# Kernel tuning notes

Hardware: AMD Instinct MI355X
Metric: run time of the kernel (lower is better)

The kernel has to match this reference:

```python
import jax, jax.numpy as jnp
import numpy as np

H1 = 768
H2 = 768
B, LQ, LK = 8, 1024, 1024


def setup_inputs() -> dict:
    key = jax.random.key(0)
    ks = jax.random.split(key, 12)
    s1 = 1.0 / np.sqrt(H1)
    s2 = 1.0 / np.sqrt(H2)
    # weights stored as [in, out] (equivalent to torch Linear weight.T)
    return {
        "tensor1": jax.random.normal(ks[0], (B, LQ, H1), jnp.float32),
        "tensor2": jax.random.normal(ks[1], (B, LK, H2), jnp.float32),
        "Wq": jax.random.uniform(ks[2], (3, H1, H2), jnp.float32, -s1, s1),
        "bq": jax.random.uniform(ks[3], (3, H2), jnp.float32, -s1, s1),
        "Wk": jax.random.uniform(ks[4], (3, H2, H2), jnp.float32, -s2, s2),
        "bk": jax.random.uniform(ks[5], (3, H2), jnp.float32, -s2, s2),
        "Wv": jax.random.uniform(ks[6], (3, H2, H2), jnp.float32, -s2, s2),
        "bv": jax.random.uniform(ks[7], (3, H2), jnp.float32, -s2, s2),
        "Wp": jax.random.uniform(ks[8], (3 * H2, H2), jnp.float32, -1.0 / np.sqrt(3 * H2), 1.0 / np.sqrt(3 * H2)),
        "bp": jax.random.uniform(ks[9], (H2,), jnp.float32, -1.0 / np.sqrt(3 * H2), 1.0 / np.sqrt(3 * H2)),
    }


def reference(tensor1, tensor2, Wq, bq, Wk, bk, Wv, bv, Wp, bp):
    # Three independent cross-attention heads, stacked on leading axis h=3.
    q = jnp.einsum("bqd,hde->hbqe", tensor1, Wq) + bq[:, None, None, :]  # [3,B,LQ,H2]
    k = jnp.einsum("bkd,hde->hbke", tensor2, Wk) + bk[:, None, None, :]  # [3,B,LK,H2]
    v = jnp.einsum("bkd,hde->hbke", tensor2, Wv) + bv[:, None, None, :]  # [3,B,LK,H2]
    scores = jnp.einsum("hbqe,hbke->hbqk", q, k)  # NOTE: no 1/sqrt(d) scaling, per original
    weights = jax.nn.softmax(scores, axis=-1)
    ctx = jnp.einsum("hbqk,hbke->hbqe", weights, v)  # [3,B,LQ,H2]
    # concat heads along feature dim -> [B,LQ,3*H2]
    multi = jnp.transpose(ctx, (1, 2, 0, 3)).reshape(ctx.shape[1], ctx.shape[2], -1)
    # project_multihead: ReLU then Linear
    return jax.nn.relu(multi) @ Wp + bp
```

## Files before the change

kernel.cpp:

```cpp
#include <hip/hip_runtime.h>
#include <hip/hip_bf16.h>


typedef _Float16 f16;
typedef __attribute__((ext_vector_type(8))) _Float16 f16x8;
typedef __attribute__((ext_vector_type(4))) float f32x4;
typedef __attribute__((ext_vector_type(4))) short s16x4;

#define DI __device__ __forceinline__

DI short f2hs(float f){
  f16 h = (f16)f;
  return __builtin_bit_cast(short, h);
}
DI float hs2f(short s){
  return (float)__builtin_bit_cast(f16, s);
}

DI f32x4 mfma16(f16x8 a, f16x8 b, f32x4 c){
  return __builtin_amdgcn_mfma_f32_16x16x32_f16(a, b, c, 0, 0, 0);
}

#define GLL16(gp, lp) __builtin_amdgcn_global_load_lds( \
    (const __attribute__((address_space(1))) unsigned int*)(gp), \
    (__attribute__((address_space(3))) unsigned int*)(lp), 16, 0, 0)

__global__ void cvt2_f16_kernel(const float* __restrict__ a, const float* __restrict__ b,
                                short* __restrict__ oa, short* __restrict__ ob, int n4each){
  int i = blockIdx.x * blockDim.x + threadIdx.x;
  const float* in = (i < n4each) ? a : b;
  short* out = (i < n4each) ? oa : ob;
  int j = (i < n4each) ? i : i - n4each;
  f32x4 v = ((const f32x4*)in)[j];
  s16x4 o;
  o[0]=f2hs(v[0]); o[1]=f2hs(v[1]); o[2]=f2hs(v[2]); o[3]=f2hs(v[3]);
  ((s16x4*)out)[j] = o;
}

__global__ void transpose2_kernel(const float* __restrict__ Wv, const float* __restrict__ Wp,
                                  short* __restrict__ WvT, short* __restrict__ WpT){
  __shared__ float tile[32][33];
  const float* in; short* out; int R, r0;
  if (blockIdx.z == 0){
    int hd = blockIdx.y / 24;
    in = Wv + (long)hd*768*768; out = WvT + (long)hd*768*768;
    R = 768; r0 = (blockIdx.y % 24) * 32;
  } else {
    in = Wp; out = WpT; R = 2304; r0 = blockIdx.y * 32;
  }
  int c0 = blockIdx.x * 32;
  int tx = threadIdx.x, ty = threadIdx.y;
  #pragma unroll
  for (int k=0;k<4;k++)
    tile[ty + k*8][tx] = in[(long)(r0 + ty + k*8) * 768 + c0 + tx];
  __syncthreads();
  #pragma unroll
  for (int k=0;k<4;k++)
    out[(long)(c0 + ty + k*8) * R + r0 + tx] = f2hs(tile[tx][ty + k*8]);
}

DI void gemm_tile64(const short* __restrict__ A, const short* __restrict__ Bt, int K,
                    int m0, int n0, short* As, short* Bs, f32x4 (&acc)[4][4])
{
  const int tid = threadIdx.x, wave = tid>>6, lane = tid&63;
  const int wm = wave>>1, wn = wave&1;
  const int fl = lane&15, fq = lane>>4;
  const int srow = lane>>2, scol = (lane&3)*8;
  for (int kk=0; kk<K; kk+=64){
    __syncthreads();
    #pragma unroll
    for (int c=0;c<2;c++)
      #pragma unroll
      for (int r=0;r<2;r++){
        const int rb = r*64 + wave*16;
        GLL16(A  + (long)(m0+rb+srow)*K + kk + c*32 + scol, As + c*4096 + rb*32);
        GLL16(Bt + (long)(n0+rb+srow)*K + kk + c*32 + scol, Bs + c*4096 + rb*32);
      }
    __syncthreads();
    #pragma unroll
    for (int c=0;c<2;c++){
      f16x8 a[4];
      #pragma unroll
      for (int i=0;i<4;i++) a[i] = *(const f16x8*)(As + c*4096 + (wm*64+i*16+fl)*32 + fq*8);
      #pragma unroll
      for (int j=0;j<4;j++){
        f16x8 b = *(const f16x8*)(Bs + c*4096 + (wn*64+j*16+fl)*32 + fq*8);
        #pragma unroll
        for (int i=0;i<4;i++) acc[i][j] = mfma16(a[i], b, acc[i][j]);
      }
    }
  }
}

__global__ __launch_bounds__(256,2) void gemm_m_kernel(
    const short* __restrict__ WqH, const short* __restrict__ WkH, short* __restrict__ Mt)
{
  __shared__ short As[8192];
  __shared__ short Bs[8192];
  const int h = blockIdx.z;
  const int m0 = blockIdx.x*128, n0 = blockIdx.y*128;
  const int tid = threadIdx.x, wave = tid>>6, lane = tid&63;
  const int wm = wave>>1, wn = wave&1;
  const int fl = lane&15, fq = lane>>4;

  f32x4 vz = {0.f,0.f,0.f,0.f};
  f32x4 acc[4][4];
  #pragma unroll
  for (int i=0;i<4;i++)
    #pragma unroll
    for (int j=0;j<4;j++) acc[i][j] = vz;

  gemm_tile64(WqH + (long)h*768*768, WkH + (long)h*768*768, 768, m0, n0, As, Bs, acc);

  short* outp = Mt + (long)h*768*768;
  #pragma unroll
  for (int j=0;j<4;j++){
    int col = n0 + wn*64 + j*16 + fl;
    #pragma unroll
    for (int i=0;i<4;i++){
      int row = m0 + wm*64 + i*16 + fq*4;
      s16x4 pack;
      #pragma unroll
      for (int r=0;r<4;r++) pack[r] = f2hs(acc[i][j][r]);
      *(s16x4*)(outp + (long)col*768 + row) = pack;
    }
  }
}

__global__ void vvec_kernel(const float* __restrict__ Wk, const float* __restrict__ bq,
                            float* __restrict__ w){
  const int h = blockIdx.x, chunk = blockIdx.y;
  const int tid = threadIdx.x, wave = tid>>6, lane = tid&63;
  const float* bql = bq + h*768 + lane*12;
  float bv[12];
  #pragma unroll
  for (int e=0;e<12;e++) bv[e] = bql[e];
  for (int r = 0; r < 24; r++){
    int d = chunk*96 + r*4 + wave;
    const float* row = Wk + ((long)h*768 + d)*768 + lane*12;
    float s = 0.f;
    #pragma unroll
    for (int e=0;e<12;e++) s += row[e] * bv[e];
    s += __shfl_xor(s, 1);
    s += __shfl_xor(s, 2);
    s += __shfl_xor(s, 4);
    s += __shfl_xor(s, 8);
    s += __shfl_xor(s, 16);
    s += __shfl_xor(s, 32);
    if (lane == 0) w[h*768 + d] = s;
  }
}

__global__ __launch_bounds__(256,2) void gemm_gv_kernel(
    const short* __restrict__ t1b, const short* __restrict__ t2b,
    const short* __restrict__ Mt, const short* __restrict__ WvT,
    const float* __restrict__ wv, const float* __restrict__ bv,
    short* __restrict__ Gb, short* __restrict__ Vtb)
{
  __shared__ short As[8192];
  __shared__ short Bs[8192];
  const int z = blockIdx.z;
  const int h = z % 3, which = z / 3;
  const short* A  = (which==0) ? t1b : t2b;
  const short* Bt = ((which==0)?Mt:WvT) + (long)h*768*768;
  const int m0 = blockIdx.x*128, n0 = blockIdx.y*128;
  const int tid = threadIdx.x, wave = tid>>6, lane = tid&63;
  const int wm = wave>>1, wn = wave&1;
  const int fl = lane&15, fq = lane>>4;

  f32x4 vz = {0.f,0.f,0.f,0.f};
  f32x4 acc[4][4];
  #pragma unroll
  for (int i=0;i<4;i++)
    #pragma unroll
    for (int j=0;j<4;j++) acc[i][j] = vz;

  gemm_tile64(A, Bt, 768, m0, n0, As, Bs, acc);

  if (which == 0){
    const float* bias = wv + h*768;
    short* outp = Gb + (long)h*8192*768;
    #pragma unroll
    for (int j=0;j<4;j++){
      int col = n0 + wn*64 + j*16 + fl;
      float bb = bias[col];
      #pragma unroll
      for (int i=0;i<4;i++){
        int row = m0 + wm*64 + i*16 + fq*4;
        #pragma unroll
        for (int r=0;r<4;r++)
          outp[(long)(row+r)*768 + col] = f2hs(acc[i][j][r] + bb);
      }
    }
  } else {
    const float* bias = bv + h*768;
    const int bidx = m0 >> 10;
    const int lk0  = m0 & 1023;
    short* outp = Vtb + (long)(h*8 + bidx)*768*1024;
    #pragma unroll
    for (int j=0;j<4;j++){
      int e = n0 + wn*64 + j*16 + fl;
      float bb = bias[e];
      #pragma unroll
      for (int i=0;i<4;i++){
        int lk = lk0 + wm*64 + i*16 + fq*4;
        s16x4 pack;
        #pragma unroll
        for (int r=0;r<4;r++) pack[r] = f2hs(acc[i][j][r] + bb);
        *(s16x4*)(outp + (long)e*1024 + lk) = pack;
      }
    }
  }
}

__global__ __launch_bounds__(256,2) void qk_exp_kernel(
    const short* __restrict__ Gb, const short* __restrict__ t2b,
    short* __restrict__ P, float* __restrict__ Mx, float* __restrict__ Lx)
{
  __shared__ short As[8192];
  __shared__ short Bs[8192];
  __shared__ float red0[2][2][64];
  __shared__ float red1[2][2][64];
  const int id = blockIdx.x;
  const int xcd = id & 7, s_ = id >> 3;
  const int hb = xcd*3 + (s_ >> 6);
  const int inner = s_ & 63;
  const int qt = inner & 7, ct = inner >> 3;
  const int h = hb >> 3, b = hb & 7;
  const int tid = threadIdx.x, wave = tid>>6, lane = tid&63;
  const int wm = wave>>1, wn = wave&1;
  const int fl = lane&15, fq = lane>>4;
  const short* Abase = Gb + ((long)h*8192 + b*1024)*768;
  const short* Bbase = t2b + (long)b*1024*768;

  f32x4 vz = {0.f,0.f,0.f,0.f};
  f32x4 acc[4][4];
  #pragma unroll
  for (int i=0;i<4;i++)
    #pragma unroll
    for (int j=0;j<4;j++) acc[i][j] = vz;

  gemm_tile64(Abase, Bbase, 768, qt*128, ct*128, As, Bs, acc);

  float mt[4][4];
  #pragma unroll
  for (int i=0;i<4;i++)
    #pragma unroll
    for (int r=0;r<4;r++){
      float m = acc[i][0][r];
      #pragma unroll
      for (int j=1;j<4;j++) m = fmaxf(m, acc[i][j][r]);
      m = fmaxf(m, __shfl_xor(m, 1));
      m = fmaxf(m, __shfl_xor(m, 2));
      m = fmaxf(m, __shfl_xor(m, 4));
      m = fmaxf(m, __shfl_xor(m, 8));
      mt[i][r] = m;
      if (fl == 0) red0[wn][wm][i*16 + fq*4 + r] = m;
    }
  __syncthreads();
  #pragma unroll
  for (int i=0;i<4;i++)
    #pragma unroll
    for (int r=0;r<4;r++)
      mt[i][r] = fmaxf(red0[0][wm][i*16 + fq*4 + r], red0[1][wm][i*16 + fq*4 + r]);

  #pragma unroll
  for (int i=0;i<4;i++)
    #pragma unroll
    for (int r=0;r<4;r++){
      float s = 0.f;
      #pragma unroll
      for (int j=0;j<4;j++){
        float p = __expf(acc[i][j][r] - mt[i][r]);
        acc[i][j][r] = p;
        s += p;
      }
      s += __shfl_xor(s, 1);
      s += __shfl_xor(s, 2);
      s += __shfl_xor(s, 4);
      s += __shfl_xor(s, 8);
      if (fl == 0) red1[wn][wm][i*16 + fq*4 + r] = s;
    }
  __syncthreads();

  #pragma unroll
  for (int j=0;j<4;j++){
    int c = ct*128 + wn*64 + j*16 + fl;
    #pragma unroll
    for (int i=0;i<4;i++){
      int q = qt*128 + wm*64 + i*16 + fq*4;
      #pragma unroll
      for (int r=0;r<4;r++)
        P[((long)hb*1024 + q + r)*1024 + c] = f2hs(acc[i][j][r]);
    }
  }
  if (fl == 0 && wn == 0){
    long aux = ((long)(hb*8 + ct))*1024 + qt*128;
    #pragma unroll
    for (int i=0;i<4;i++)
      #pragma unroll
      for (int r=0;r<4;r++){
        int row = wm*64 + i*16 + fq*4 + r;
        Mx[aux + row] = mt[i][r];
        Lx[aux + row] = red1[0][wm][row & 63] + red1[1][wm][row & 63];
      }
  }
}

__global__ __launch_bounds__(256,2) void pv_kernel(
    const short* __restrict__ P, const short* __restrict__ Vtb,
    const float* __restrict__ Mx, const float* __restrict__ Lx, short* __restrict__ multi)
{
  __shared__ short As[8192];
  __shared__ short Bs[8192];
  __shared__ float scl[8][128];
  const int id = blockIdx.x;
  const int xcd = id & 7, s_ = id >> 3;
  const int hb = xcd*3 + s_/48;
  const int inner = s_ % 48;
  const int qt = inner & 7, et = inner >> 3;
  const int h = hb >> 3, b = hb & 7;
  const int tid = threadIdx.x, wave = tid>>6, lane = tid&63;
  const int wm = wave>>1, wn = wave&1;
  const int fl = lane&15, fq = lane>>4;
  const int srow = lane>>2, scol = (lane&3)*8;
  const short* Abase = P + (long)hb*1024*1024 + (long)(qt*128)*1024;
  const short* Bbase = Vtb + (long)hb*768*1024 + (long)(et*128)*1024;

  if (tid < 128){
    long a0 = ((long)(hb*8))*1024 + qt*128 + tid;
    float m[8], l[8];
    #pragma unroll
    for (int t=0;t<8;t++){ m[t] = Mx[a0 + t*1024]; l[t] = Lx[a0 + t*1024]; }
    float mg = m[0];
    #pragma unroll
    for (int t=1;t<8;t++) mg = fmaxf(mg, m[t]);
    float lg = 0.f;
    #pragma unroll
    for (int t=0;t<8;t++) lg += l[t] * __expf(m[t] - mg);
    float inv = 1.0f / lg;
    #pragma unroll
    for (int t=0;t<8;t++) scl[t][tid] = __expf(m[t] - mg) * inv;
  }
  __syncthreads();

  f32x4 vz = {0.f,0.f,0.f,0.f};
  f32x4 acc[4][4];
  #pragma unroll
  for (int i=0;i<4;i++)
    #pragma unroll
    for (int j=0;j<4;j++) acc[i][j] = vz;

  for (int ct=0; ct<8; ct++){
    f16 s[4];
    #pragma unroll
    for (int i=0;i<4;i++) s[i] = (f16)scl[ct][wm*64 + i*16 + fl];
    #pragma unroll
    for (int t=0;t<2;t++){
      const int kk = ct*128 + t*64;
      __syncthreads();
      #pragma unroll
      for (int c=0;c<2;c++)
        #pragma unroll
        for (int r=0;r<2;r++){
          const int rb = r*64 + wave*16;
          GLL16(Abase + (long)(rb+srow)*1024 + kk + c*32 + scol, As + c*4096 + rb*32);
          GLL16(Bbase + (long)(rb+srow)*1024 + kk + c*32 + scol, Bs + c*4096 + rb*32);
        }
      __syncthreads();
      #pragma unroll
      for (int c=0;c<2;c++){
        f16x8 a[4];
        #pragma unroll
        for (int i=0;i<4;i++){
          f16x8 av = *(const f16x8*)(As + c*4096 + (wm*64+i*16+fl)*32 + fq*8);
          f16x8 sv;
          #pragma unroll
          for (int e=0;e<8;e++) sv[e] = s[i];
          a[i] = av * sv;
        }
        #pragma unroll
        for (int j=0;j<4;j++){
          f16x8 bvv = *(const f16x8*)(Bs + c*4096 + (wn*64+j*16+fl)*32 + fq*8);
          #pragma unroll
          for (int i=0;i<4;i++) acc[i][j] = mfma16(a[i], bvv, acc[i][j]);
        }
      }
    }
  }

  short* mp = multi + (long)(b*1024 + qt*128)*2304 + h*768 + et*128;
  #pragma unroll
  for (int j=0;j<4;j++){
    int e = wn*64 + j*16 + fl;
    #pragma unroll
    for (int i=0;i<4;i++){
      int q = wm*64 + i*16 + fq*4;
      #pragma unroll
      for (int r=0;r<4;r++)
        mp[(long)(q+r)*2304 + e] = f2hs(fmaxf(acc[i][j][r], 0.f));
    }
  }
}

__global__ __launch_bounds__(256,2) void gemm_out_kernel(
    const short* __restrict__ A, const short* __restrict__ Bt,
    const float* __restrict__ bias, float* __restrict__ out)
{
  __shared__ short As[8192];
  __shared__ short Bs[8192];
  const int m0 = blockIdx.x*128, n0 = blockIdx.y*128;
  const int tid = threadIdx.x, wave = tid>>6, lane = tid&63;
  const int wm = wave>>1, wn = wave&1;
  const int fl = lane&15, fq = lane>>4;

  f32x4 vz = {0.f,0.f,0.f,0.f};
  f32x4 acc[4][4];
  #pragma unroll
  for (int i=0;i<4;i++)
    #pragma unroll
    for (int j=0;j<4;j++) acc[i][j] = vz;

  gemm_tile64(A, Bt, 2304, m0, n0, As, Bs, acc);

  #pragma unroll
  for (int j=0;j<4;j++){
    int col = n0 + wn*64 + j*16 + fl;
    float bb = bias[col];
    #pragma unroll
    for (int i=0;i<4;i++){
      int row = m0 + wm*64 + i*16 + fq*4;
      #pragma unroll
      for (int r=0;r<4;r++)
        out[(long)(row+r)*768 + col] = acc[i][j][r] + bb;
    }
  }
}

extern "C" void kernel_launch(void* const* d_in, const int* in_sizes, int n_in,
                              void* d_out, int out_size, void* d_ws, size_t ws_size,
                              hipStream_t stream)
{
  const float* t1 = (const float*)d_in[0];
  const float* t2 = (const float*)d_in[1];
  const float* Wq = (const float*)d_in[2];
  const float* bq = (const float*)d_in[3];
  const float* Wk = (const float*)d_in[4];
  const float* Wv = (const float*)d_in[6];
  const float* bv = (const float*)d_in[7];
  const float* Wp = (const float*)d_in[8];
  const float* bp = (const float*)d_in[9];
  float* out = (float*)d_out;

  char* ws = (char*)d_ws;
  size_t off = 0;
  auto carve = [&](size_t bytes){ void* p = ws + off; off += (bytes + 255) & ~(size_t)255; return p; };
  short* t1b = (short*)carve(8L*1024*768*2);
  short* t2b = (short*)carve(8L*1024*768*2);
  short* WqH = (short*)carve(3L*768*768*2);
  short* WkH = (short*)carve(3L*768*768*2);
  short* WvT = (short*)carve(3L*768*768*2);
  short* WpT = (short*)carve(768L*2304*2);
  short* Mt  = (short*)carve(3L*768*768*2);
  short* Gb  = (short*)carve(3L*8192*768*2);
  short* Vtb = (short*)carve(3L*8*768*1024*2);
  short* Pb  = (short*)carve(24L*1024*1024*2);
  float* Mx  = (float*)carve(24L*8*1024*4);
  float* Lx  = (float*)carve(24L*8*1024*4);
  float* wvb = (float*)carve(3L*768*4);
  short* multib = Gb;

  cvt2_f16_kernel<<<12288, 256, 0, stream>>>(t1, t2, t1b, t2b, 1572864);
  cvt2_f16_kernel<<<3456, 256, 0, stream>>>(Wq, Wk, WqH, WkH, 442368);
  transpose2_kernel<<<dim3(24,72,2), dim3(32,8), 0, stream>>>(Wv, Wp, WvT, WpT);
  vvec_kernel<<<dim3(3,8), 256, 0, stream>>>(Wk, bq, wvb);
  gemm_m_kernel<<<dim3(6,6,3), 256, 0, stream>>>(WqH, WkH, Mt);
  gemm_gv_kernel<<<dim3(64,6,6), 256, 0, stream>>>(t1b, t2b, Mt, WvT, wvb, bv, Gb, Vtb);
  qk_exp_kernel<<<1536, 256, 0, stream>>>(Gb, t2b, Pb, Mx, Lx);
  pv_kernel<<<1152, 256, 0, stream>>>(Pb, Vtb, Mx, Lx, multib);
  gemm_out_kernel<<<dim3(64,6,1), 256, 0, stream>>>(multib, WpT, bp, out);
}
```

Baseline: 399.4 us.

## Use 256x256 tiles with 4-stage async LDS pipeline in G/V projection GEMM

Replaces the 128x128 tile G/V projection GEMM with a 512-thread 256x256 tile kernel. Each wave now computes a 128x64 sub-tile. Operands are loaded into LDS through a 4-deep ring of direct global-to-LDS loads with XOR swizzling, explicit vmcnt waits and raised MFMA priority. The larger tiles raise arithmetic intensity and the prefetch hides load latency, at the cost of more LDS (128KB per block) and more registers, plus fewer blocks (576) to spread across CUs.

```diff
diff --git a/kernel.cpp b/kernel.cpp
--- a/kernel.cpp
+++ b/kernel.cpp
@@ -151,31 +151,85 @@
   }
 }
 
-__global__ __launch_bounds__(256,2) void gemm_gv_kernel(
+__global__ __launch_bounds__(512,2) void gemm_gv256_kernel(
     const short* __restrict__ t1b, const short* __restrict__ t2b,
     const short* __restrict__ Mt, const short* __restrict__ WvT,
     const float* __restrict__ wv, const float* __restrict__ bv,
     short* __restrict__ Gb, short* __restrict__ Vtb)
 {
-  __shared__ short As[8192];
-  __shared__ short Bs[8192];
+  __shared__ short As4[4][8192];
+  __shared__ short Bs4[4][8192];
+
   const int z = blockIdx.z;
   const int h = z % 3, which = z / 3;
   const short* A  = (which==0) ? t1b : t2b;
   const short* Bt = ((which==0)?Mt:WvT) + (long)h*768*768;
-  const int m0 = blockIdx.x*128, n0 = blockIdx.y*128;
-  const int tid = threadIdx.x, wave = tid>>6, lane = tid&63;
-  const int wm = wave>>1, wn = wave&1;
+  const int m0 = blockIdx.x*256, n0 = blockIdx.y*256;
+  const int tid = threadIdx.x, wave = tid>>6, lane = tid&63;
+  const int wm = wave>>2, wn = wave&3;
   const int fl = lane&15, fq = lane>>4;
 
+  const int lr = lane>>2;
+  const int ss = ((lane&3) ^ ((lane>>3)&3)) * 8;
+  const int rs = (fq ^ ((fl>>1)&3)) * 8;
+
   f32x4 vz = {0.f,0.f,0.f,0.f};
-  f32x4 acc[4][4];
-  #pragma unroll
-  for (int i=0;i<4;i++)
+  f32x4 acc[8][4];
+  #pragma unroll
+  for (int i=0;i<8;i++)
     #pragma unroll
     for (int j=0;j<4;j++) acc[i][j] = vz;
 
-  gemm_tile64(A, Bt, 768, m0, n0, As, Bs, acc);
+  auto STAGE = [&](int rg, int s){
+    const int kk = s*32;
+    #pragma unroll
+    for (int g=0; g<2; g++){
+      const int rb = g*128 + wave*16;
+      GLL16(A  + (long)(m0+rb+lr)*768 + kk + ss, &As4[rg][rb*32]);
+      GLL16(Bt + (long)(n0+rb+lr)*768 + kk + ss, &Bs4[rg][rb*32]);
+    }
+  };
+
+  auto COMPUTE = [&](int rg){
+    const short* Ab = &As4[rg][0];
+    const short* Bb = &Bs4[rg][0];
+    f16x8 b[4];
+    #pragma unroll
+    for (int j=0;j<4;j++)
+      b[j] = *(const f16x8*)(Bb + (wn*64 + j*16 + fl)*32 + rs);
+    #pragma unroll
+    for (int mq=0; mq<2; mq++){
+      f16x8 a[4];
+      #pragma unroll
+      for (int i=0;i<4;i++)
+        a[i] = *(const f16x8*)(Ab + (wm*128 + mq*64 + i*16 + fl)*32 + rs);
+      __builtin_amdgcn_s_setprio(1);
+      #pragma unroll
+      for (int j=0;j<4;j++)
+        #pragma unroll
+        for (int i=0;i<4;i++)
+          acc[mq*4+i][j] = mfma16(a[i], b[j], acc[mq*4+i][j]);
+      __builtin_amdgcn_s_setprio(0);
+    }
+  };
+
+  STAGE(0, 0);
+  STAGE(1, 1);
+  asm volatile("s_waitcnt vmcnt(4)" ::: "memory");
+  __builtin_amdgcn_s_barrier();
+
+  for (int s = 0; s < 22; ++s){
+    STAGE((s+2)&3, s+2);
+    asm volatile("s_waitcnt vmcnt(8)" ::: "memory");
+    __builtin_amdgcn_s_barrier();
+    COMPUTE(s&3);
+  }
+  asm volatile("s_waitcnt vmcnt(4)" ::: "memory");
+  __builtin_amdgcn_s_barrier();
+  COMPUTE(22&3);
+  asm volatile("s_waitcnt vmcnt(0)" ::: "memory");
+  __builtin_amdgcn_s_barrier();
+  COMPUTE(23&3);
 
   if (which == 0){
     const float* bias = wv + h*768;
@@ -185,8 +239,8 @@
       int col = n0 + wn*64 + j*16 + fl;
       float bb = bias[col];
       #pragma unroll
-      for (int i=0;i<4;i++){
-        int row = m0 + wm*64 + i*16 + fq*4;
+      for (int i=0;i<8;i++){
+        int row = m0 + wm*128 + i*16 + fq*4;
         #pragma unroll
         for (int r=0;r<4;r++)
           outp[(long)(row+r)*768 + col] = f2hs(acc[i][j][r] + bb);
@@ -202,8 +256,8 @@
       int e = n0 + wn*64 + j*16 + fl;
       float bb = bias[e];
       #pragma unroll
-      for (int i=0;i<4;i++){
-        int lk = lk0 + wm*64 + i*16 + fq*4;
+      for (int i=0;i<8;i++){
+        int lk = lk0 + wm*128 + i*16 + fq*4;
         s16x4 pack;
         #pragma unroll
         for (int r=0;r<4;r++) pack[r] = f2hs(acc[i][j][r] + bb);
@@ -475,7 +529,7 @@
   transpose2_kernel<<<dim3(24,72,2), dim3(32,8), 0, stream>>>(Wv, Wp, WvT, WpT);
   vvec_kernel<<<dim3(3,8), 256, 0, stream>>>(Wk, bq, wvb);
   gemm_m_kernel<<<dim3(6,6,3), 256, 0, stream>>>(WqH, WkH, Mt);
-  gemm_gv_kernel<<<dim3(64,6,6), 256, 0, stream>>>(t1b, t2b, Mt, WvT, wvb, bv, Gb, Vtb);
+  gemm_gv256_kernel<<<dim3(32,3,6), 512, 0, stream>>>(t1b, t2b, Mt, WvT, wvb, bv, Gb, Vtb);
   qk_exp_kernel<<<1536, 256, 0, stream>>>(Gb, t2b, Pb, Mx, Lx);
   pv_kernel<<<1152, 256, 0, stream>>>(Pb, Vtb, Mx, Lx, multib);
   gemm_out_kernel<<<dim3(64,6,1), 256, 0, stream>>>(multib, WpT, bp, out);
```

Measured after the change: 413.3 us. 3.5% more time.

## Fuse preprocessing kernels into one launch and XOR-swizzle LDS tiles

Applied to the files above, without the earlier changes.

Merges the four preprocessing kernels (activation and weight casts, the Wv/Wp transposes, and the bias-vector reduction) into one block-indexed launch to cut launch gaps and tail effects. It also applies an XOR swizzle to the LDS column chunk, both in the global_load_lds writes and in the fragment reads of gemm_tile64 and pv_kernel, to reduce LDS bank conflicts. The fused kernel declares the transpose's shared tile for every block, and the vvec branch now shares a launch with many small blocks. Swizzle correctness depends on the write and read mappings matching.

```diff
diff --git a/kernel.cpp b/kernel.cpp
--- a/kernel.cpp
+++ b/kernel.cpp
@@ -25,38 +25,88 @@
     (const __attribute__((address_space(1))) unsigned int*)(gp), \
     (__attribute__((address_space(3))) unsigned int*)(lp), 16, 0, 0)
 
-__global__ void cvt2_f16_kernel(const float* __restrict__ a, const float* __restrict__ b,
-                                short* __restrict__ oa, short* __restrict__ ob, int n4each){
-  int i = blockIdx.x * blockDim.x + threadIdx.x;
-  const float* in = (i < n4each) ? a : b;
-  short* out = (i < n4each) ? oa : ob;
-  int j = (i < n4each) ? i : i - n4each;
-  f32x4 v = ((const f32x4*)in)[j];
-  s16x4 o;
-  o[0]=f2hs(v[0]); o[1]=f2hs(v[1]); o[2]=f2hs(v[2]); o[3]=f2hs(v[3]);
-  ((s16x4*)out)[j] = o;
-}
-
-__global__ void transpose2_kernel(const float* __restrict__ Wv, const float* __restrict__ Wp,
-                                  short* __restrict__ WvT, short* __restrict__ WpT){
+__global__ void pre_fused_kernel(
+    const float* __restrict__ t1, const float* __restrict__ t2,
+    short* __restrict__ t1b, short* __restrict__ t2b,
+    const float* __restrict__ Wq, const float* __restrict__ Wk,
+    short* __restrict__ WqH, short* __restrict__ WkH,
+    const float* __restrict__ Wv, const float* __restrict__ Wp,
+    short* __restrict__ WvT, short* __restrict__ WpT,
+    const float* __restrict__ bq, float* __restrict__ wvb)
+{
   __shared__ float tile[32][33];
-  const float* in; short* out; int R, r0;
-  if (blockIdx.z == 0){
-    int hd = blockIdx.y / 24;
-    in = Wv + (long)hd*768*768; out = WvT + (long)hd*768*768;
-    R = 768; r0 = (blockIdx.y % 24) * 32;
-  } else {
-    in = Wp; out = WpT; R = 2304; r0 = blockIdx.y * 32;
-  }
-  int c0 = blockIdx.x * 32;
-  int tx = threadIdx.x, ty = threadIdx.y;
-  #pragma unroll
-  for (int k=0;k<4;k++)
-    tile[ty + k*8][tx] = in[(long)(r0 + ty + k*8) * 768 + c0 + tx];
-  __syncthreads();
-  #pragma unroll
-  for (int k=0;k<4;k++)
-    out[(long)(c0 + ty + k*8) * R + r0 + tx] = f2hs(tile[tx][ty + k*8]);
+  int bid = blockIdx.x;
+  const int tid = threadIdx.x;
+
+  if (bid < 12288){
+    int i = bid*256 + tid;
+    const float* in = (i < 1572864) ? t1 : t2;
+    short* out = (i < 1572864) ? t1b : t2b;
+    int j = (i < 1572864) ? i : i - 1572864;
+    f32x4 v = ((const f32x4*)in)[j];
+    s16x4 o;
+    o[0]=f2hs(v[0]); o[1]=f2hs(v[1]); o[2]=f2hs(v[2]); o[3]=f2hs(v[3]);
+    ((s16x4*)out)[j] = o;
+    return;
+  }
+  bid -= 12288;
+  if (bid < 3456){
+    int i = bid*256 + tid;
+    const float* in = (i < 442368) ? Wq : Wk;
+    short* out = (i < 442368) ? WqH : WkH;
+    int j = (i < 442368) ? i : i - 442368;
+    f32x4 v = ((const f32x4*)in)[j];
+    s16x4 o;
+    o[0]=f2hs(v[0]); o[1]=f2hs(v[1]); o[2]=f2hs(v[2]); o[3]=f2hs(v[3]);
+    ((s16x4*)out)[j] = o;
+    return;
+  }
+  bid -= 3456;
+  if (bid < 3456){
+    const int bz = bid / 1728, rem = bid % 1728;
+    const int by = rem / 24, bx = rem % 24;
+    const float* in; short* out; int R, r0;
+    if (bz == 0){
+      int hd = by / 24;
+      in = Wv + (long)hd*768*768; out = WvT + (long)hd*768*768;
+      R = 768; r0 = (by % 24) * 32;
+    } else {
+      in = Wp; out = WpT; R = 2304; r0 = by * 32;
+    }
+    int c0 = bx * 32;
+    int tx = tid & 31, ty = tid >> 5;
+    #pragma unroll
+    for (int k=0;k<4;k++)
+      tile[ty + k*8][tx] = in[(long)(r0 + ty + k*8) * 768 + c0 + tx];
+    __syncthreads();
+    #pragma unroll
+    for (int k=0;k<4;k++)
+      out[(long)(c0 + ty + k*8) * R + r0 + tx] = f2hs(tile[tx][ty + k*8]);
+    return;
+  }
+  bid -= 3456;
+  {
+    const int h = bid / 8, chunk = bid % 8;
+    const int wave = tid>>6, lane = tid&63;
+    const float* bql = bq + h*768 + lane*12;
+    float bv[12];
+    #pragma unroll
+    for (int e=0;e<12;e++) bv[e] = bql[e];
+    for (int r = 0; r < 24; r++){
+      int d = chunk*96 + r*4 + wave;
+      const float* row = Wk + ((long)h*768 + d)*768 + lane*12;
+      float s = 0.f;
+      #pragma unroll
+      for (int e=0;e<12;e++) s += row[e] * bv[e];
+      s += __shfl_xor(s, 1);
+      s += __shfl_xor(s, 2);
+      s += __shfl_xor(s, 4);
+      s += __shfl_xor(s, 8);
+      s += __shfl_xor(s, 16);
+      s += __shfl_xor(s, 32);
+      if (lane == 0) wvb[h*768 + d] = s;
+    }
+  }
 }
 
 DI void gemm_tile64(const short* __restrict__ A, const short* __restrict__ Bt, int K,
@@ -65,7 +115,9 @@
   const int tid = threadIdx.x, wave = tid>>6, lane = tid&63;
   const int wm = wave>>1, wn = wave&1;
   const int fl = lane&15, fq = lane>>4;
-  const int srow = lane>>2, scol = (lane&3)*8;
+  const int srow = lane>>2;
+  const int scol = ((lane&3) ^ ((lane>>3)&3))*8;
+  const int rs   = (fq ^ ((fl>>1)&3))*8;
   for (int kk=0; kk<K; kk+=64){
     __syncthreads();
     #pragma unroll
@@ -81,10 +133,10 @@
     for (int c=0;c<2;c++){
       f16x8 a[4];
       #pragma unroll
-      for (int i=0;i<4;i++) a[i] = *(const f16x8*)(As + c*4096 + (wm*64+i*16+fl)*32 + fq*8);
+      for (int i=0;i<4;i++) a[i] = *(const f16x8*)(As + c*4096 + (wm*64+i*16+fl)*32 + rs);
       #pragma unroll
       for (int j=0;j<4;j++){
-        f16x8 b = *(const f16x8*)(Bs + c*4096 + (wn*64+j*16+fl)*32 + fq*8);
+        f16x8 b = *(const f16x8*)(Bs + c*4096 + (wn*64+j*16+fl)*32 + rs);
         #pragma unroll
         for (int i=0;i<4;i++) acc[i][j] = mfma16(a[i], b, acc[i][j]);
       }
@@ -124,30 +176,6 @@
       for (int r=0;r<4;r++) pack[r] = f2hs(acc[i][j][r]);
       *(s16x4*)(outp + (long)col*768 + row) = pack;
     }
-  }
-}
-
-__global__ void vvec_kernel(const float* __restrict__ Wk, const float* __restrict__ bq,
-                            float* __restrict__ w){
-  const int h = blockIdx.x, chunk = blockIdx.y;
-  const int tid = threadIdx.x, wave = tid>>6, lane = tid&63;
-  const float* bql = bq + h*768 + lane*12;
-  float bv[12];
-  #pragma unroll
-  for (int e=0;e<12;e++) bv[e] = bql[e];
-  for (int r = 0; r < 24; r++){
-    int d = chunk*96 + r*4 + wave;
-    const float* row = Wk + ((long)h*768 + d)*768 + lane*12;
-    float s = 0.f;
-    #pragma unroll
-    for (int e=0;e<12;e++) s += row[e] * bv[e];
-    s += __shfl_xor(s, 1);
-    s += __shfl_xor(s, 2);
-    s += __shfl_xor(s, 4);
-    s += __shfl_xor(s, 8);
-    s += __shfl_xor(s, 16);
-    s += __shfl_xor(s, 32);
-    if (lane == 0) w[h*768 + d] = s;
   }
 }
 
@@ -323,7 +351,9 @@
   const int tid = threadIdx.x, wave = tid>>6, lane = tid&63;
   const int wm = wave>>1, wn = wave&1;
   const int fl = lane&15, fq = lane>>4;
-  const int srow = lane>>2, scol = (lane&3)*8;
+  const int srow = lane>>2;
+  const int scol = ((lane&3) ^ ((lane>>3)&3))*8;
+  const int rs   = (fq ^ ((fl>>1)&3))*8;
   const short* Abase = P + (long)hb*1024*1024 + (long)(qt*128)*1024;
   const short* Bbase = Vtb + (long)hb*768*1024 + (long)(et*128)*1024;
 
@@ -373,7 +403,7 @@
         f16x8 a[4];
         #pragma unroll
         for (int i=0;i<4;i++){
-          f16x8 av = *(const f16x8*)(As + c*4096 + (wm*64+i*16+fl)*32 + fq*8);
+          f16x8 av = *(const f16x8*)(As + c*4096 + (wm*64+i*16+fl)*32 + rs);
           f16x8 sv;
           #pragma unroll
           for (int e=0;e<8;e++) sv[e] = s[i];
@@ -381,7 +411,7 @@
         }
         #pragma unroll
         for (int j=0;j<4;j++){
-          f16x8 bvv = *(const f16x8*)(Bs + c*4096 + (wn*64+j*16+fl)*32 + fq*8);
+          f16x8 bvv = *(const f16x8*)(Bs + c*4096 + (wn*64+j*16+fl)*32 + rs);
           #pragma unroll
           for (int i=0;i<4;i++) acc[i][j] = mfma16(a[i], bvv, acc[i][j]);
         }
@@ -470,10 +500,8 @@
   float* wvb = (float*)carve(3L*768*4);
   short* multib = Gb;
 
-  cvt2_f16_kernel<<<12288, 256, 0, stream>>>(t1, t2, t1b, t2b, 1572864);
-  cvt2_f16_kernel<<<3456, 256, 0, stream>>>(Wq, Wk, WqH, WkH, 442368);
-  transpose2_kernel<<<dim3(24,72,2), dim3(32,8), 0, stream>>>(Wv, Wp, WvT, WpT);
-  vvec_kernel<<<dim3(3,8), 256, 0, stream>>>(Wk, bq, wvb);
+  pre_fused_kernel<<<19224, 256, 0, stream>>>(t1, t2, t1b, t2b, Wq, Wk, WqH, WkH,
+                                              Wv, Wp, WvT, WpT, bq, wvb);
   gemm_m_kernel<<<dim3(6,6,3), 256, 0, stream>>>(WqH, WkH, Mt);
   gemm_gv_kernel<<<dim3(64,6,6), 256, 0, stream>>>(t1b, t2b, Mt, WvT, wvb, bv, Gb, Vtb);
   qk_exp_kernel<<<1536, 256, 0, stream>>>(Gb, t2b, Pb, Mx, Lx);
```

After: 382.7 us. -4.2%, faster.
